# Kernel tuning notes

Hardware: AMD Instinct MI355X
Metric: run time of the kernel (lower is better)

Reference implementation:

```python
import jax, jax.numpy as jnp
import numpy as np

H = 16          # num_attention_heads
D_MODEL = 2048  # hidden_size
HEAD_DIM = D_MODEL // H  # 128
B, S = 4, 2048


def setup_inputs() -> dict:
    key = jax.random.key(0)
    ks = jax.random.split(key, 9)
    std = D_MODEL ** -0.5
    hidden_states = jax.random.normal(ks[0], (B, S, D_MODEL), dtype=jnp.float32)
    q_w = jax.random.normal(ks[1], (H * HEAD_DIM, D_MODEL), dtype=jnp.float32) * std
    k_w = jax.random.normal(ks[2], (HEAD_DIM, D_MODEL), dtype=jnp.float32) * std
    v_w = jax.random.normal(ks[3], (HEAD_DIM, D_MODEL), dtype=jnp.float32) * std
    o_w = jax.random.normal(ks[4], (D_MODEL, H * HEAD_DIM), dtype=jnp.float32) * std
    q_b = jnp.zeros((H * HEAD_DIM,), dtype=jnp.float32)
    k_b = jnp.zeros((HEAD_DIM,), dtype=jnp.float32)
    v_b = jnp.zeros((HEAD_DIM,), dtype=jnp.float32)
    o_b = jnp.zeros((D_MODEL,), dtype=jnp.float32)
    return {"hidden_states": hidden_states, "q_w": q_w, "q_b": q_b,
            "k_w": k_w, "k_b": k_b, "v_w": v_w, "v_b": v_b,
            "o_w": o_w, "o_b": o_b}


def reference(hidden_states, q_w, q_b, k_w, k_b, v_w, v_b, o_w, o_b):
    b, s, _ = hidden_states.shape
    # projections: q -> H heads, k/v -> single shared KV head (MQA)
    q = (hidden_states @ q_w.T + q_b).reshape(b, s, H, HEAD_DIM)   # bshd
    k = hidden_states @ k_w.T + k_b                                 # bkd (1 kv head)
    v = hidden_states @ v_w.T + v_b                                 # bkd
    # QK^T with KV head broadcast across all query heads
    scores = jnp.einsum('bqhd,bkd->bhqk', q, k) / (HEAD_DIM ** 0.5)
    # causal mask (triu above diagonal)
    causal = jnp.triu(jnp.ones((s, s), dtype=bool), k=1)
    scores = jnp.where(causal[None, None], -jnp.inf, scores)
    # softmax in fp32, cast back to input dtype
    attn = jax.nn.softmax(scores.astype(jnp.float32), axis=-1).astype(q.dtype)
    out = jnp.einsum('bhqk,bkd->bqhd', attn, v).reshape(b, s, H * HEAD_DIM)
    return out @ o_w.T + o_b
```

## Files before the change

kernel.cpp:

```cpp
#include <hip/hip_runtime.h>
#include <stdint.h>

typedef __bf16 bf16;
typedef __bf16 bf16x4 __attribute__((ext_vector_type(4)));
typedef __bf16 bf16x8 __attribute__((ext_vector_type(8)));
typedef float f32x4 __attribute__((ext_vector_type(4)));
typedef short s16x4 __attribute__((ext_vector_type(4)));

using gp_t = __attribute__((address_space(1))) const void*;
using lp_t = __attribute__((address_space(3))) void*;

__device__ __forceinline__ void gld16(const void* g, void* l) {
  __builtin_amdgcn_global_load_lds((gp_t)g, (lp_t)l, 16, 0, 0);
}

struct CvtSegs {
  const float* src[10];
  bf16* dst[10];
  int cnt[10];
  int n;
};

__global__ void cvt_kernel(CvtSegs segs) {
  const int stride = gridDim.x * blockDim.x;
  const int t0 = blockIdx.x * blockDim.x + threadIdx.x;
  for (int s = 0; s < segs.n; s++) {
    const float4* src = (const float4*)segs.src[s];
    bf16x4* dst = (bf16x4*)segs.dst[s];
    int cnt4 = segs.cnt[s] >> 2;
    for (int idx = t0; idx < cnt4; idx += stride) {
      float4 v = src[idx];
      bf16x4 o; o[0] = (bf16)v.x; o[1] = (bf16)v.y; o[2] = (bf16)v.z; o[3] = (bf16)v.w;
      dst[idx] = o;
    }
  }
}

__global__ __launch_bounds__(512, 2)
void gemm256(const bf16* __restrict__ A, const bf16* __restrict__ W,
             const bf16* __restrict__ bias, void* __restrict__ Cv,
             void* __restrict__ Cv2, void* __restrict__ Cv3,
             int N, int K, int store_sel)
{
  __shared__ __align__(16) bf16 As[2][256 * 64];
  __shared__ __align__(16) bf16 Bs[2][256 * 64];
  const int tid  = threadIdx.x;
  const int lane = tid & 63;
  const int w    = tid >> 6;
  const int wm   = w >> 2, wn = w & 3;
  const int quad = lane >> 4, l16 = lane & 15;
  const int m0 = blockIdx.x * 256, n0 = blockIdx.y * 256;

  f32x4 acc[8][4] = {};

  auto stageAB = [&](int buf, int k0, int itbase) {
#pragma unroll
    for (int it = itbase; it < itbase + 2; it++) {
      int c   = tid + it * 512;
      int row = c >> 3;
      int cc  = (c & 7) ^ (row & 7);
      gld16(A + (size_t)(m0 + row) * K + k0 + cc * 8, &As[buf][c * 8]);
      gld16(W + (size_t)(n0 + row) * K + k0 + cc * 8, &Bs[buf][c * 8]);
    }
  };

  stageAB(0, 0, 0);
  stageAB(0, 0, 2);
  __syncthreads();
  __builtin_amdgcn_sched_barrier(0);

  int cur = 0;
  for (int k0 = 0; k0 < K; k0 += 64) {
    const bool nxt = (k0 + 64 < K);
    bf16x8 bw[4][2];
#pragma unroll
    for (int p = 0; p < 4; p++) {
      if (nxt && p < 2) stageAB(cur ^ 1, k0 + 64, p * 2);
      if (p == 0) {
#pragma unroll
        for (int nj = 0; nj < 4; nj++)
#pragma unroll
          for (int dk = 0; dk < 2; dk++) {
            int row = wn * 64 + nj * 16 + l16;
            bw[nj][dk] = *(const bf16x8*)&Bs[cur][(row * 8 + ((dk * 4 + quad) ^ (row & 7))) * 8];
          }
      }
      bf16x8 af[2][2];
#pragma unroll
      for (int mi = 0; mi < 2; mi++)
#pragma unroll
        for (int dk = 0; dk < 2; dk++) {
          int row = wm * 128 + (p * 2 + mi) * 16 + l16;
          af[mi][dk] = *(const bf16x8*)&As[cur][(row * 8 + ((dk * 4 + quad) ^ (row & 7))) * 8];
        }
      __builtin_amdgcn_s_barrier();
      __builtin_amdgcn_sched_barrier(0);
      __builtin_amdgcn_s_setprio(1);
#pragma unroll
      for (int dk = 0; dk < 2; dk++)
#pragma unroll
        for (int mi = 0; mi < 2; mi++)
#pragma unroll
          for (int nj = 0; nj < 4; nj++)
            acc[p * 2 + mi][nj] = __builtin_amdgcn_mfma_f32_16x16x32_bf16(
                af[mi][dk], bw[nj][dk], acc[p * 2 + mi][nj], 0, 0, 0);
      __builtin_amdgcn_s_setprio(0);
      if (p == 3) asm volatile("s_waitcnt vmcnt(0)" ::: "memory");
      __builtin_amdgcn_s_barrier();
      __builtin_amdgcn_sched_barrier(0);
    }
    cur ^= 1;
  }

#pragma unroll
  for (int nj = 0; nj < 4; nj++) {
    int col = n0 + wn * 64 + nj * 16 + l16;
    float bv = (float)bias[col];
#pragma unroll
    for (int mi = 0; mi < 8; mi++) {
#pragma unroll
      for (int r = 0; r < 4; r++) {
        int row = m0 + wm * 128 + mi * 16 + quad * 4 + r;
        float v = acc[mi][nj][r] + bv;
        if (store_sel == 2) {
          ((float*)Cv)[(size_t)row * N + col] = v;
        } else {
          if (col < 2048) {
            ((bf16*)Cv)[(size_t)row * 2048 + col] = (bf16)v;
          } else if (col < 2176) {
            ((bf16*)Cv2)[(size_t)row * 128 + (col - 2048)] = (bf16)v;
          } else {
            int b = row >> 11, s = row & 2047;
            ((bf16*)Cv3)[((size_t)(b * 128 + (col - 2176))) * 2048 + s] = (bf16)v;
          }
        }
      }
    }
  }
}

__global__ __launch_bounds__(256, 2)
void gemm_bt_f32w(const bf16* __restrict__ A, const float* __restrict__ Wf,
                  const float* __restrict__ biasf, float* __restrict__ C,
                  int M, int N, int K)
{
  __shared__ __align__(16) bf16 As[128 * 64];
  __shared__ __align__(16) bf16 Bs[128 * 64];
  const int tid  = threadIdx.x;
  const int lane = tid & 63;
  const int w    = tid >> 6;
  const int wm   = w >> 1, wn = w & 1;
  const int quad = lane >> 4, l16 = lane & 15;
  const int m0 = blockIdx.x * 128, n0 = blockIdx.y * 128;

  f32x4 acc[4][4] = {};

  for (int k0 = 0; k0 < K; k0 += 64) {
#pragma unroll
    for (int it = 0; it < 4; it++) {
      int c = tid + it * 256;
      int row = c >> 3;
      int cc  = (c & 7) ^ (row & 7);
      gld16(A + (size_t)(m0 + row) * K + k0 + cc * 8, &As[c * 8]);
      size_t woff = (size_t)(n0 + row) * K + k0 + cc * 8;
      float4 x0 = *(const float4*)(Wf + woff);
      float4 x1 = *(const float4*)(Wf + woff + 4);
      bf16x8 v;
      v[0] = (bf16)x0.x; v[1] = (bf16)x0.y; v[2] = (bf16)x0.z; v[3] = (bf16)x0.w;
      v[4] = (bf16)x1.x; v[5] = (bf16)x1.y; v[6] = (bf16)x1.z; v[7] = (bf16)x1.w;
      *(bf16x8*)&Bs[c * 8] = v;
    }
    __syncthreads();
#pragma unroll
    for (int dk = 0; dk < 2; dk++) {
      bf16x8 af[4], bw[4];
#pragma unroll
      for (int i = 0; i < 4; i++) {
        int row = wm * 64 + i * 16 + l16;
        af[i] = *(const bf16x8*)&As[(row * 8 + ((dk * 4 + quad) ^ (row & 7))) * 8];
      }
#pragma unroll
      for (int j = 0; j < 4; j++) {
        int row = wn * 64 + j * 16 + l16;
        bw[j] = *(const bf16x8*)&Bs[(row * 8 + ((dk * 4 + quad) ^ (row & 7))) * 8];
      }
#pragma unroll
      for (int i = 0; i < 4; i++)
#pragma unroll
        for (int j = 0; j < 4; j++)
          acc[i][j] = __builtin_amdgcn_mfma_f32_16x16x32_bf16(af[i], bw[j], acc[i][j], 0, 0, 0);
    }
    __syncthreads();
  }

#pragma unroll
  for (int j = 0; j < 4; j++) {
    int col = n0 + wn * 64 + j * 16 + l16;
    float bv = biasf[col];
#pragma unroll
    for (int i = 0; i < 4; i++)
#pragma unroll
      for (int r = 0; r < 4; r++) {
        int row = m0 + wm * 64 + i * 16 + quad * 4 + r;
        C[(size_t)row * N + col] = acc[i][j][r] + bv;
      }
  }
}

__global__ __launch_bounds__(256, 2)
void mqa_attn(const bf16* Qg, const bf16* __restrict__ Kg,
              const bf16* __restrict__ Vtg, bf16* AO)
{
  __shared__ __align__(16) bf16 Ks[2][64 * 128];
  __shared__ __align__(16) bf16 Vs[2][128 * 64];

  const int tid  = threadIdx.x;
  const int lane = tid & 63;
  const int w    = tid >> 6;
  const int quad = lane >> 4, l16 = lane & 15;
  const int rb   = w * 32;
  const int bh = blockIdx.y;
  const int b  = bh >> 4, h = bh & 15;
  const float C2  = 0.12751879526288147f;
  const float NEG = -3.0e4f;

  for (int half = 0; half < 2; half++) {
    const int qi = half ? (15 - (int)blockIdx.x) : (int)blockIdx.x;
    const int q0 = qi * 128;

    bf16x8 aq[2][4];
    {
      const bf16* qb = Qg + ((size_t)(b * 2048 + q0 + rb + l16)) * 2048 + h * 128 + quad * 8;
#pragma unroll
      for (int i = 0; i < 2; i++)
#pragma unroll
        for (int dk = 0; dk < 4; dk++)
          aq[i][dk] = *(const bf16x8*)(qb + (size_t)i * 16 * 2048 + dk * 32);
    }

    float m_reg[2] = {NEG, NEG};
    float l_reg[2] = {0.0f, 0.0f};
    f32x4 ot[2][8] = {};

    const int nt = 2 * qi + 2;

#pragma unroll
    for (int it = 0; it < 4; it++) {
      int c = tid + it * 256;
      int rk = c >> 4, ck = (c & 15) ^ (rk & 15);
      gld16(Kg + ((size_t)(b * 2048 + rk)) * 128 + ck * 8, &Ks[0][c * 8]);
      int rv = c >> 3, cv = (c & 7) ^ (rv & 7);
      gld16(Vtg + ((size_t)(b * 128 + rv)) * 2048 + cv * 8, &Vs[0][c * 8]);
    }
    __syncthreads();

    int cur = 0;
    for (int kt = 0; kt < nt; kt++) {
      const int kk0 = kt * 64;

      if (kt + 1 < nt) {
        const int nk0 = kk0 + 64;
#pragma unroll
        for (int it = 0; it < 4; it++) {
          int c = tid + it * 256;
          int rk = c >> 4, ck = (c & 15) ^ (rk & 15);
          gld16(Kg + ((size_t)(b * 2048 + nk0 + rk)) * 128 + ck * 8, &Ks[cur ^ 1][c * 8]);
          int rv = c >> 3, cv = (c & 7) ^ (rv & 7);
          gld16(Vtg + ((size_t)(b * 128 + rv)) * 2048 + nk0 + cv * 8, &Vs[cur ^ 1][c * 8]);
        }
      }

      if (kk0 <= q0 + rb + 31) {
        f32x4 st[4][2] = {};
#pragma unroll
        for (int dk = 0; dk < 4; dk++) {
          bf16x8 bk[4];
#pragma unroll
          for (int j = 0; j < 4; j++) {
            int row = j * 16 + l16;
            bk[j] = *(const bf16x8*)&Ks[cur][(row * 16 + ((dk * 4 + quad) ^ (row & 15))) * 8];
          }
          __builtin_amdgcn_s_setprio(1);
#pragma unroll
          for (int j = 0; j < 4; j++)
#pragma unroll
            for (int i = 0; i < 2; i++)
              st[j][i] = __builtin_amdgcn_mfma_f32_16x16x32_bf16(bk[j], aq[i][dk], st[j][i], 0, 0, 0);
          __builtin_amdgcn_s_setprio(0);
        }

        if (kk0 + 63 > q0 + rb) {
#pragma unroll
          for (int j = 0; j < 4; j++)
#pragma unroll
            for (int i = 0; i < 2; i++)
#pragma unroll
              for (int r = 0; r < 4; r++) {
                int key = kk0 + j * 16 + quad * 4 + r;
                int qg  = q0 + rb + i * 16 + l16;
                if (key > qg) st[j][i][r] = NEG;
              }
        }

        s16x4 ps[2][4];
#pragma unroll
        for (int i = 0; i < 2; i++) {
          float mx = st[0][i][0];
#pragma unroll
          for (int j = 0; j < 4; j++)
#pragma unroll
            for (int r = 0; r < 4; r++) mx = fmaxf(mx, st[j][i][r]);
          mx = fmaxf(mx, __shfl_xor(mx, 16, 64));
          mx = fmaxf(mx, __shfl_xor(mx, 32, 64));
          float mo = m_reg[i];
          if (__any(mx > mo)) {
            float mn = fmaxf(mo, mx);
            float al = exp2f((mo - mn) * C2);
            l_reg[i] *= al;
#pragma unroll
            for (int jd = 0; jd < 8; jd++)
#pragma unroll
              for (int r = 0; r < 4; r++) ot[i][jd][r] *= al;
            m_reg[i] = mn;
          }
          float mc = m_reg[i] * C2;
          float rs = 0.0f;
#pragma unroll
          for (int j = 0; j < 4; j++) {
            float p0 = exp2f(st[j][i][0] * C2 - mc);
            float p1 = exp2f(st[j][i][1] * C2 - mc);
            float p2 = exp2f(st[j][i][2] * C2 - mc);
            float p3 = exp2f(st[j][i][3] * C2 - mc);
            rs += (p0 + p1) + (p2 + p3);
            union { bf16x4 h; s16x4 s; } pu;
            pu.h[0] = (bf16)p0; pu.h[1] = (bf16)p1;
            pu.h[2] = (bf16)p2; pu.h[3] = (bf16)p3;
            ps[i][j] = pu.s;
          }
          rs += __shfl_xor(rs, 16, 64);
          rs += __shfl_xor(rs, 32, 64);
          l_reg[i] += rs;
        }

#pragma unroll
        for (int jd = 0; jd < 8; jd++) {
          int vrow = jd * 16 + l16;
          s16x4 vf[4];
#pragma unroll
          for (int jk = 0; jk < 4; jk++) {
            int vch = (jk * 2 + (quad >> 1)) ^ (vrow & 7);
            vf[jk] = *(const s16x4*)&Vs[cur][(vrow * 8 + vch) * 8 + (quad & 1) * 4];
          }
          __builtin_amdgcn_s_setprio(1);
#pragma unroll
          for (int jk = 0; jk < 4; jk++)
#pragma unroll
            for (int i = 0; i < 2; i++)
              ot[i][jd] = __builtin_amdgcn_mfma_f32_16x16x16bf16_1k(vf[jk], ps[i][jk], ot[i][jd], 0, 0, 0);
          __builtin_amdgcn_s_setprio(0);
        }
      }
      __syncthreads();
      cur ^= 1;
    }

#pragma unroll
    for (int i = 0; i < 2; i++) {
      float l = l_reg[i];
      float inv = (l > 0.0f) ? 1.0f / l : 0.0f;
      size_t base = ((size_t)(b * 2048 + q0 + rb + i * 16 + l16)) * 2048 + h * 128 + quad * 4;
#pragma unroll
      for (int jd = 0; jd < 8; jd++) {
        bf16x4 ov;
#pragma unroll
        for (int r = 0; r < 4; r++) ov[r] = (bf16)(ot[i][jd][r] * inv);
        *(bf16x4*)(AO + base + jd * 16) = ov;
      }
    }
  }
}

extern "C" void kernel_launch(void* const* d_in, const int* in_sizes, int n_in,
                              void* d_out, int out_size, void* d_ws, size_t ws_size,
                              hipStream_t stream)
{
  const float* X   = (const float*)d_in[0];
  const float* q_w = (const float*)d_in[1];
  const float* q_b = (const float*)d_in[2];
  const float* k_w = (const float*)d_in[3];
  const float* k_b = (const float*)d_in[4];
  const float* v_w = (const float*)d_in[5];
  const float* v_b = (const float*)d_in[6];
  const float* o_w = (const float*)d_in[7];
  const float* o_b = (const float*)d_in[8];

  char* outc = (char*)d_out;
  bf16* Xb    = (bf16*)(outc);
  bf16* Kg    = (bf16*)(outc + 33554432);
  bf16* Vtg   = (bf16*)(outc + 35651584);
  bf16* wq_b  = (bf16*)(outc + 37748736);
  bf16* wkv_b = (bf16*)(outc + 46137344);
  bf16* qb_b  = (bf16*)(outc + 47185920);
  bf16* kvb_b = (bf16*)(outc + 47190016);

  bf16* Qg = (bf16*)d_ws;
  bf16* AO = Qg;

  const bool big_ws = ws_size >= (size_t)(33554432 + 8388608 + 8192);
  bf16* wo_b = big_ws ? (bf16*)((char*)d_ws + 33554432) : nullptr;
  bf16* ob_b = big_ws ? (bf16*)((char*)d_ws + 41943040) : nullptr;

  CvtSegs segs;
  int n = 0;
  segs.src[n] = X;   segs.dst[n] = Xb;            segs.cnt[n] = 16777216; n++;
  segs.src[n] = q_w; segs.dst[n] = wq_b;          segs.cnt[n] = 4194304;  n++;
  segs.src[n] = k_w; segs.dst[n] = wkv_b;         segs.cnt[n] = 262144;   n++;
  segs.src[n] = v_w; segs.dst[n] = wkv_b + 262144; segs.cnt[n] = 262144;  n++;
  segs.src[n] = q_b; segs.dst[n] = qb_b;          segs.cnt[n] = 2048;     n++;
  segs.src[n] = k_b; segs.dst[n] = kvb_b;         segs.cnt[n] = 128;      n++;
  segs.src[n] = v_b; segs.dst[n] = kvb_b + 128;   segs.cnt[n] = 128;      n++;
  if (big_ws) {
    segs.src[n] = o_w; segs.dst[n] = wo_b;        segs.cnt[n] = 4194304;  n++;
    segs.src[n] = o_b; segs.dst[n] = ob_b;        segs.cnt[n] = 2048;     n++;
  }
  segs.n = n;

  cvt_kernel<<<dim3(1024), dim3(256), 0, stream>>>(segs);
  gemm256<<<dim3(32, 9), dim3(512), 0, stream>>>(Xb, wq_b, qb_b, Qg, Kg, Vtg,
                                                 2304, 2048, 4);
  mqa_attn<<<dim3(8, 64), dim3(256), 0, stream>>>(Qg, Kg, Vtg, AO);
  if (big_ws)
    gemm256<<<dim3(32, 8), dim3(512), 0, stream>>>(AO, wo_b, ob_b, d_out,
                                                   nullptr, nullptr, 2048, 2048, 2);
  else
    gemm_bt_f32w<<<dim3(64, 16), dim3(256), 0, stream>>>(AO, o_w, o_b, (float*)d_out,
                                                         8192, 2048, 2048);
}
```

Measured before the change: 558.0 us.

## Use 4-stage K=32 LDS pipeline with XCD-aware block swizzle in GEMM

Replaces the double-buffered K=64 tile loop in the 256x256 GEMM with a four-buffer K=32 ring that keeps three tiles of global->LDS loads in flight, using partial vmcnt waits and one barrier per step. It also remaps block indices so blocks on the same XCD share A row panels, aiming for better L2 reuse, and changes launch bounds to one block per CU. The intent is to hide global load latency and cut barrier overhead. The block remap hardcodes a 32-wide grid.x and the waitcnt counts assume exactly four loads per stage, so other shapes or grids could break it.

After: 546.9 us. -2.0%, faster.

```diff
diff --git a/kernel.cpp b/kernel.cpp
--- a/kernel.cpp
+++ b/kernel.cpp
@@ -36,80 +36,80 @@
   }
 }
 
-__global__ __launch_bounds__(512, 2)
+__global__ __launch_bounds__(512, 1)
 void gemm256(const bf16* __restrict__ A, const bf16* __restrict__ W,
              const bf16* __restrict__ bias, void* __restrict__ Cv,
              void* __restrict__ Cv2, void* __restrict__ Cv3,
              int N, int K, int store_sel)
 {
-  __shared__ __align__(16) bf16 As[2][256 * 64];
-  __shared__ __align__(16) bf16 Bs[2][256 * 64];
+  __shared__ __align__(16) bf16 As[4][256 * 32];
+  __shared__ __align__(16) bf16 Bs[4][256 * 32];
   const int tid  = threadIdx.x;
   const int lane = tid & 63;
   const int w    = tid >> 6;
   const int wm   = w >> 2, wn = w & 3;
   const int quad = lane >> 4, l16 = lane & 15;
-  const int m0 = blockIdx.x * 256, n0 = blockIdx.y * 256;
+
+  const int bid = (int)blockIdx.x + 32 * (int)blockIdx.y;
+  const int xcd = bid & 7, t8 = bid >> 3;
+  const int m0 = (xcd * 4 + (t8 & 3)) * 256;
+  const int n0 = (t8 >> 2) * 256;
 
   f32x4 acc[8][4] = {};
 
-  auto stageAB = [&](int buf, int k0, int itbase) {
-#pragma unroll
-    for (int it = itbase; it < itbase + 2; it++) {
+  auto stage = [&](int buf, int k0) {
+#pragma unroll
+    for (int it = 0; it < 2; it++) {
       int c   = tid + it * 512;
-      int row = c >> 3;
-      int cc  = (c & 7) ^ (row & 7);
+      int row = c >> 2;
+      int cc  = (c & 3) ^ ((row >> 1) & 3);
       gld16(A + (size_t)(m0 + row) * K + k0 + cc * 8, &As[buf][c * 8]);
       gld16(W + (size_t)(n0 + row) * K + k0 + cc * 8, &Bs[buf][c * 8]);
     }
   };
 
-  stageAB(0, 0, 0);
-  stageAB(0, 0, 2);
-  __syncthreads();
+  const int nT = K >> 5;
+
+  stage(0, 0); stage(1, 32); stage(2, 64);
+  asm volatile("s_waitcnt vmcnt(8)" ::: "memory");
+  __builtin_amdgcn_s_barrier();
   __builtin_amdgcn_sched_barrier(0);
 
-  int cur = 0;
-  for (int k0 = 0; k0 < K; k0 += 64) {
-    const bool nxt = (k0 + 64 < K);
-    bf16x8 bw[4][2];
-#pragma unroll
-    for (int p = 0; p < 4; p++) {
-      if (nxt && p < 2) stageAB(cur ^ 1, k0 + 64, p * 2);
-      if (p == 0) {
-#pragma unroll
-        for (int nj = 0; nj < 4; nj++)
-#pragma unroll
-          for (int dk = 0; dk < 2; dk++) {
-            int row = wn * 64 + nj * 16 + l16;
-            bw[nj][dk] = *(const bf16x8*)&Bs[cur][(row * 8 + ((dk * 4 + quad) ^ (row & 7))) * 8];
-          }
-      }
-      bf16x8 af[2][2];
-#pragma unroll
-      for (int mi = 0; mi < 2; mi++)
-#pragma unroll
-        for (int dk = 0; dk < 2; dk++) {
-          int row = wm * 128 + (p * 2 + mi) * 16 + l16;
-          af[mi][dk] = *(const bf16x8*)&As[cur][(row * 8 + ((dk * 4 + quad) ^ (row & 7))) * 8];
-        }
+  for (int t = 0; t < nT; t++) {
+    const int buf = t & 3;
+    if (t + 3 < nT) stage((t + 3) & 3, (t + 3) << 5);
+
+    bf16x8 bw[4];
+#pragma unroll
+    for (int j = 0; j < 4; j++) {
+      int row = wn * 64 + j * 16 + l16;
+      bw[j] = *(const bf16x8*)&Bs[buf][(row * 4 + (quad ^ ((row >> 1) & 3))) * 8];
+    }
+#pragma unroll
+    for (int h = 0; h < 2; h++) {
+      bf16x8 af[4];
+#pragma unroll
+      for (int i = 0; i < 4; i++) {
+        int row = wm * 128 + (h * 4 + i) * 16 + l16;
+        af[i] = *(const bf16x8*)&As[buf][(row * 4 + (quad ^ ((row >> 1) & 3))) * 8];
+      }
+      __builtin_amdgcn_s_setprio(1);
+#pragma unroll
+      for (int i = 0; i < 4; i++)
+#pragma unroll
+        for (int j = 0; j < 4; j++)
+          acc[h * 4 + i][j] = __builtin_amdgcn_mfma_f32_16x16x32_bf16(
+              af[i], bw[j], acc[h * 4 + i][j], 0, 0, 0);
+      __builtin_amdgcn_s_setprio(0);
+    }
+
+    if (t < nT - 3)       asm volatile("s_waitcnt vmcnt(8)" ::: "memory");
+    else if (t == nT - 3) asm volatile("s_waitcnt vmcnt(4)" ::: "memory");
+    else if (t == nT - 2) asm volatile("s_waitcnt vmcnt(0)" ::: "memory");
+    if (t < nT - 1) {
       __builtin_amdgcn_s_barrier();
       __builtin_amdgcn_sched_barrier(0);
-      __builtin_amdgcn_s_setprio(1);
-#pragma unroll
-      for (int dk = 0; dk < 2; dk++)
-#pragma unroll
-        for (int mi = 0; mi < 2; mi++)
-#pragma unroll
-          for (int nj = 0; nj < 4; nj++)
-            acc[p * 2 + mi][nj] = __builtin_amdgcn_mfma_f32_16x16x32_bf16(
-                af[mi][dk], bw[nj][dk], acc[p * 2 + mi][nj], 0, 0, 0);
-      __builtin_amdgcn_s_setprio(0);
-      if (p == 3) asm volatile("s_waitcnt vmcnt(0)" ::: "memory");
-      __builtin_amdgcn_s_barrier();
-      __builtin_amdgcn_sched_barrier(0);
-    }
-    cur ^= 1;
+    }
   }
 
 #pragma unroll
```
